# Kernel tuning notes

Measured on AMD Instinct MI355X. Metric: run time of the kernel, lower is better.

## Reference

```python
import jax, jax.numpy as jnp
import numpy as np

D, H, DK, L, FF = 512, 8, 64, 6, 2048
MAXREL = 512
R = 2 * MAXREL + 1
B, S = 4, 512


def _ln(x, g, b):
    m = jnp.mean(x, -1, keepdims=True)
    v = jnp.mean((x - m) ** 2, -1, keepdims=True)
    return (x - m) * jax.lax.rsqrt(v + 1e-5) * g + b


def _gelu(x):
    return jax.nn.gelu(x, approximate=False)


def setup_inputs() -> dict:
    key = jax.random.key(0)
    ks = iter(jax.random.split(key, 64))
    def rnd(shape, scale=0.02):
        return jax.random.normal(next(ks), shape, jnp.float32) * scale
    inp = {"x": jax.random.normal(next(ks), (B, S, D), jnp.float32)}
    # SeasonalDecomposition params (3 seasonal nets stacked on leading axis)
    inp.update(
        sd_t1_w=rnd((D, D)), sd_t1_b=jnp.zeros((D,), jnp.float32),
        sd_t2_w=rnd((D, D)), sd_t2_b=jnp.zeros((D,), jnp.float32),
        sd_s1_w=rnd((3, D, D // 2)), sd_s1_b=jnp.zeros((3, D // 2), jnp.float32),
        sd_s2_w=rnd((3, D // 2, D)), sd_s2_b=jnp.zeros((3, D), jnp.float32),
        sd_r1_w=rnd((D, D // 2)), sd_r1_b=jnp.zeros((D // 2,), jnp.float32),
        sd_r2_w=rnd((D // 2, D)), sd_r2_b=jnp.zeros((D,), jnp.float32),
        sd_comb=jnp.ones((5,), jnp.float32),
        # 6 TemporalFusionTransformer layers, params stacked on leading axis L
        wq=rnd((L, D, D)), wk=rnd((L, D, D)), wv=rnd((L, D, D)),
        wo_w=rnd((L, D, D)), wo_b=jnp.zeros((L, D), jnp.float32),
        rel_k=rnd((L, R, DK), 1.0), rel_v=rnd((L, R, DK), 1.0),
        ln_attn_g=jnp.ones((L, D), jnp.float32), ln_attn_b=jnp.zeros((L, D), jnp.float32),
        ff1_w=rnd((L, D, FF)), ff1_b=jnp.zeros((L, FF), jnp.float32),
        ff2_w=rnd((L, FF, D)), ff2_b=jnp.zeros((L, D), jnp.float32),
        n1_g=jnp.ones((L, D), jnp.float32), n1_b=jnp.zeros((L, D), jnp.float32),
        n2_g=jnp.ones((L, D), jnp.float32), n2_b=jnp.zeros((L, D), jnp.float32),
    )
    return inp


def _forward(x, sd_t1_w, sd_t1_b, sd_t2_w, sd_t2_b, sd_s1_w, sd_s1_b, sd_s2_w, sd_s2_b,
             sd_r1_w, sd_r1_b, sd_r2_w, sd_r2_b, sd_comb,
             wq, wk, wv, wo_w, wo_b, rel_k, rel_v, ln_attn_g, ln_attn_b,
             ff1_w, ff1_b, ff2_w, ff2_b, n1_g, n1_b, n2_g, n2_b):
    b, s, d = x.shape
    # relative position index matrix, rp[i, j] = clip(j - i) + MAXREL
    r = jnp.arange(s)
    rp = jnp.clip(r[None, :] - r[:, None], -MAXREL, MAXREL) + MAXREL  # [S, S]

    # ---- SeasonalDecomposition (eval mode: dropout = identity) ----
    trend = _gelu(x @ sd_t1_w + sd_t1_b) @ sd_t2_w + sd_t2_b
    h = _gelu(jnp.einsum('bsd,kdm->kbsm', x, sd_s1_w) + sd_s1_b[:, None, None, :])
    seas = jnp.einsum('kbsm,kmd->kbsd', h, sd_s2_w) + sd_s2_b[:, None, None, :]  # [3,B,S,D]
    resid = _gelu(x @ sd_r1_w + sd_r1_b) @ sd_r2_w + sd_r2_b
    w = jax.nn.softmax(sd_comb)
    x = w[0] * trend + w[4] * resid + jnp.einsum('k,kbsd->bsd', w[1:4], seas)

    scale = np.float32(1.0 / np.sqrt(DK))

    def layer(xc, p):
        q = (xc @ p['wq']).reshape(b, s, H, DK).transpose(0, 2, 1, 3)  # [B,H,S,DK]
        k = (xc @ p['wk']).reshape(b, s, H, DK).transpose(0, 2, 1, 3)
        v = (xc @ p['wv']).reshape(b, s, H, DK).transpose(0, 2, 1, 3)
        scores = jnp.einsum('bhid,bhjd->bhij', q, k) * scale
        rk = p['rel_k'][rp]  # [S,S,DK] gathered rel-pos key bias
        scores = scores + jnp.einsum('bhid,ijd->bhij', q, rk)
        a = jax.nn.softmax(scores, axis=-1)
        ctx = jnp.einsum('bhij,bhjd->bhid', a, v)
        rv = p['rel_v'][rp]  # [S,S,DK]
        ctx = ctx + jnp.einsum('bhij,ijd->bhid', a, rv)
        ctx = ctx.transpose(0, 2, 1, 3).reshape(b, s, d)
        out = ctx @ p['wo_w'] + p['wo_b']
        attn = _ln(out + xc, p['ln_attn_g'], p['ln_attn_b'])
        y = _ln(xc + attn, p['n1_g'], p['n1_b'])
        ff = _gelu(y @ p['ff1_w'] + p['ff1_b']) @ p['ff2_w'] + p['ff2_b']
        y = _ln(y + ff, p['n2_g'], p['n2_b'])
        return y, None

    layers = dict(wq=wq, wk=wk, wv=wv, wo_w=wo_w, wo_b=wo_b, rel_k=rel_k, rel_v=rel_v,
                  ln_attn_g=ln_attn_g, ln_attn_b=ln_attn_b,
                  ff1_w=ff1_w, ff1_b=ff1_b, ff2_w=ff2_w, ff2_b=ff2_b,
                  n1_g=n1_g, n1_b=n1_b, n2_g=n2_g, n2_b=n2_b)
    x, _ = jax.lax.scan(layer, x, layers)
    return x


def reference(x, sd_t1_w, sd_t1_b, sd_t2_w, sd_t2_b, sd_s1_w, sd_s1_b, sd_s2_w, sd_s2_b,
              sd_r1_w, sd_r1_b, sd_r2_w, sd_r2_b, sd_comb,
              wq, wk, wv, wo_w, wo_b, rel_k, rel_v, ln_attn_g, ln_attn_b,
              ff1_w, ff1_b, ff2_w, ff2_b, n1_g, n1_b, n2_g, n2_b):
    return _forward(x, sd_t1_w, sd_t1_b, sd_t2_w, sd_t2_b, sd_s1_w, sd_s1_b, sd_s2_w, sd_s2_b,
                    sd_r1_w, sd_r1_b, sd_r2_w, sd_r2_b, sd_comb,
                    wq, wk, wv, wo_w, wo_b, rel_k, rel_v, ln_attn_g, ln_attn_b,
                    ff1_w, ff1_b, ff2_w, ff2_b, n1_g, n1_b, n2_g, n2_b)
```

## Files before the change

kernel.cpp:

```cpp
#include <hip/hip_runtime.h>
#include <hip/hip_bf16.h>

typedef __attribute__((ext_vector_type(4))) float f32x4;
typedef __attribute__((ext_vector_type(8))) short bf16x8;
typedef __attribute__((ext_vector_type(4))) short bf16x4;

#define NL 6

static __device__ __forceinline__ unsigned short f2bf(float f) {
    __hip_bfloat16 h = __float2bfloat16(f);
    return *reinterpret_cast<unsigned short*>(&h);
}
static __device__ __forceinline__ float bf2f(unsigned short u) {
    union { unsigned int u32; float f; } c; c.u32 = ((unsigned int)u) << 16; return c.f;
}
static __device__ __forceinline__ float gelu_exact(float v) {
    return 0.5f * v * (1.0f + erff(v * 0.70710678118654752f));
}
static __device__ __forceinline__ void gload_lds16(const void* g, void* l) {
    __builtin_amdgcn_global_load_lds((const __attribute__((address_space(1))) void*)g,
                                     (__attribute__((address_space(3))) void*)l, 16, 0, 0);
}
static __device__ __forceinline__ f32x4 MF(bf16x8 a, bf16x8 b, f32x4 c) {
    return __builtin_amdgcn_mfma_f32_16x16x32_bf16(a, b, c, 0, 0, 0);
}

template<int BM, int BN, bool OBF, bool BIAS, bool GACT, bool SPART, bool DUAL, bool VTR>
__global__ __launch_bounds__(256)
void gemm3(const unsigned short* __restrict__ A, const unsigned short* __restrict__ B,
           void* __restrict__ C, unsigned short* __restrict__ C2,
           const float* __restrict__ bias,
           int M, int N, int nkt, int skN, int lda, int ldb, int ldc, float alpha,
           int modA, long sA1, long sA2, int modB, long sB1, long sB2,
           int modC, long sC1, long sC2, int biasStride, long pStride)
{
    constexpr int MI = BM / 32, NI = BN / 32;
    constexpr int ACH = BM / 8, NCH = (BM + BN) / 8;
    constexpr int HALF = (BM + BN) * 64;
    __shared__ __attribute__((aligned(16))) unsigned short Ls[2 * HALF];

    const int bz = blockIdx.z;
    const int sk = SPART ? (bz % skN) : 0;
    const int z  = SPART ? (bz / skN) : bz;
    const unsigned short* Ab = A + (long)(z % modA) * sA1 + (long)(z / modA) * sA2;
    const unsigned short* Bb = B + (long)(z % modB) * sB1 + (long)(z / modB) * sB2;
    const long offC = (long)(z % modC) * sC1 + (long)(z / modC) * sC2;

    const int bm0 = blockIdx.x * BM, bn0 = blockIdx.y * BN;
    const int t = threadIdx.x, lane = t & 63, w = t >> 6;
    const int wm = (w >> 1) * (BM / 2), wn = (w & 1) * (BN / 2);
    const int crow8 = lane >> 3, cs8 = lane & 7;
    const int fr = lane & 15, kq = lane >> 4;
    const int kBase = sk * nkt * 64;

    auto stagef = [&](int kt, int sb) {
        const int k0 = kBase + (kt << 6);
        const int base = sb * HALF;
        #pragma unroll
        for (int c0 = 0; c0 < NCH; c0 += 4) {
            int c = c0 + w;
            if (c < NCH) {
                const unsigned short* gp;
                if (c < ACH) {
                    int rit = c * 8 + crow8;
                    int ks = cs8 ^ (rit & 7);
                    gp = Ab + (long)(bm0 + rit) * lda + k0 + ks * 8;
                } else {
                    int rit = (c - ACH) * 8 + crow8;
                    int ks = cs8 ^ (rit & 7);
                    gp = Bb + (long)(bn0 + rit) * ldb + k0 + ks * 8;
                }
                gload_lds16(gp, &Ls[base + c * 512]);
            }
        }
    };

    f32x4 acc[MI][NI];
    #pragma unroll
    for (int a = 0; a < MI; a++)
        #pragma unroll
        for (int b = 0; b < NI; b++) acc[a][b] = (f32x4){0.f, 0.f, 0.f, 0.f};

    stagef(0, 0);
    __syncthreads();

    for (int kt = 0; kt < nkt; ++kt) {
        const int sb = kt & 1;
        const int base = sb * HALF;
        if (kt + 1 < nkt) stagef(kt + 1, sb ^ 1);
        bf16x8 af[2][MI], bfr[2][NI];
        #pragma unroll
        for (int mi = 0; mi < MI; mi++) {
            int R = wm + mi * 16 + fr;
            af[0][mi] = *(const bf16x8*)&Ls[base + R * 64 + ((kq ^ (R & 7)) << 3)];
            af[1][mi] = *(const bf16x8*)&Ls[base + R * 64 + (((4 + kq) ^ (R & 7)) << 3)];
        }
        #pragma unroll
        for (int ni = 0; ni < NI; ni++) {
            int Rb = wn + ni * 16 + fr;
            bfr[0][ni] = *(const bf16x8*)&Ls[base + BM * 64 + Rb * 64 + ((kq ^ (Rb & 7)) << 3)];
            bfr[1][ni] = *(const bf16x8*)&Ls[base + BM * 64 + Rb * 64 + (((4 + kq) ^ (Rb & 7)) << 3)];
        }
        #pragma unroll
        for (int kh = 0; kh < 2; kh++)
            #pragma unroll
            for (int mi = 0; mi < MI; mi++)
                #pragma unroll
                for (int ni = 0; ni < NI; ni++)
                    acc[mi][ni] = MF(af[kh][mi], bfr[kh][ni], acc[mi][ni]);
        __syncthreads();
    }

    const int q4 = (lane >> 4) << 2;
    if (VTR && bn0 >= 1024) {
        #pragma unroll
        for (int mi = 0; mi < MI; mi++)
            #pragma unroll
            for (int ni = 0; ni < NI; ni++)
                #pragma unroll
                for (int j = 0; j < 4; j++) {
                    int lr = wm + mi * 16 + q4 + j;
                    int lc = wn + ni * 16 + fr;
                    Ls[lc * 64 + ((((lr >> 4) ^ (lc & 3)) << 4) | (lr & 15))] = f2bf(acc[mi][ni][j]);
                }
        __syncthreads();
        int dl = t >> 2, c4 = (t & 3) << 4;
        const unsigned short* src = &Ls[dl * 64 + (((t & 3) ^ (dl & 3)) << 4)];
        unsigned short* dst = C2 + ((long)((bm0 >> 9) * 8 + ((bn0 - 1024) >> 6)) * 64 + dl) * 512
                              + (bm0 & 511) + c4;
        *(bf16x8*)dst = *(const bf16x8*)src;
        *((bf16x8*)dst + 1) = *((const bf16x8*)src + 1);
    } else if (SPART) {
        float* P = (float*)C + sk * pStride + offC;
        #pragma unroll
        for (int mi = 0; mi < MI; mi++)
            #pragma unroll
            for (int ni = 0; ni < NI; ni++)
                #pragma unroll
                for (int j = 0; j < 4; j++) {
                    int gr = bm0 + wm + mi * 16 + q4 + j;
                    int gc = bn0 + wn + ni * 16 + fr;
                    if (gc < N) P[(long)gr * ldc + gc] = acc[mi][ni][j] * alpha;
                }
    } else {
        float* Cf = (float*)C + offC;
        unsigned short* Ch = (unsigned short*)C + offC;
        unsigned short* C2h = DUAL ? (C2 + offC) : nullptr;
        const float* bp = BIAS ? (bias + (long)z * biasStride) : nullptr;
        #pragma unroll
        for (int mi = 0; mi < MI; mi++)
            #pragma unroll
            for (int ni = 0; ni < NI; ni++)
                #pragma unroll
                for (int j = 0; j < 4; j++) {
                    int gr = bm0 + wm + mi * 16 + q4 + j;
                    int gc = bn0 + wn + ni * 16 + fr;
                    if (gc < N) {
                        float v = acc[mi][ni][j] * alpha;
                        if (BIAS) v += bp[gc];
                        if (GACT) v = gelu_exact(v);
                        if (OBF) Ch[(long)gr * ldc + gc] = f2bf(v);
                        else     Cf[(long)gr * ldc + gc] = v;
                        if (DUAL) C2h[(long)gr * ldc + gc] = f2bf(v);
                    }
                }
    }
}

__global__ __launch_bounds__(256)
void fused_attn4(const unsigned short* __restrict__ qkv,
                 const unsigned short* __restrict__ vt,
                 const unsigned short* __restrict__ rk,
                 const unsigned short* __restrict__ rvt,
                 float* __restrict__ op, float* __restrict__ ml)
{
    __shared__ __attribute__((aligned(16))) unsigned short L[40960];
    const int bh = blockIdx.y, b = bh >> 3, h = bh & 7;
    const int i0 = blockIdx.x * 64;
    const int half = blockIdx.z;
    const int t = threadIdx.x, lane = t & 63, wv = t >> 6;
    const int crow = lane >> 2, cs = lane & 3;
    const int fr = lane & 15, kq = lane >> 4;
    const int q4 = kq << 2;
    const int iiw = wv * 16;
    const int PB = 28672, GA = 32768;

    const unsigned short* Qg = qkv + ((long)(b * 512 + i0)) * 1536 + h * 64;
    const unsigned short* Kg = qkv + ((long)(b * 512)) * 1536 + 512 + h * 64;
    const unsigned short* Vg = vt + ((long)bh * 64) * 512;

    auto stage = [&](int jt) {
        const int j0 = jt * 64, rbase = j0 - i0 + 448;
        #pragma unroll
        for (int k = 0; k < 12; k++) {
            int c = wv + k * 4;
            const unsigned short* gp; int dst;
            if (c < 8) {
                int kt = c >> 2, row = (c & 3) * 16 + crow, ks = cs ^ (row & 3);
                gp = Kg + (long)(j0 + row) * 1536 + kt * 32 + ks * 8;
                dst = 4096 + c * 512;
            } else if (c < 16) {
                int cc = c - 8;
                int kt = cc >> 2, row = (cc & 3) * 16 + crow, ks = cs ^ (row & 3);
                gp = Vg + (long)row * 512 + j0 + kt * 32 + ks * 8;
                dst = 8192 + cc * 512;
            } else if (c < 32) {
                int cc = c - 16;
                int kt = cc >> 2, row = (cc & 3) * 16 + crow, ks = cs ^ (row & 3);
                gp = rvt + (long)row * 1056 + rbase + kt * 32 + ks * 8;
                dst = 12288 + cc * 512;
            } else {
                int cc = c - 32;
                int kt = cc >> 3, row = (cc & 7) * 16 + crow, ks = cs ^ (row & 3);
                gp = rk + (long)(rbase + row) * 64 + kt * 32 + ks * 8;
                dst = 20480 + cc * 512;
            }
            gload_lds16(gp, &L[dst]);
        }
    };

    #pragma unroll
    for (int k = 0; k < 2; k++) {
        int c = wv + k * 4;
        int kt = c >> 2, row = (c & 3) * 16 + crow, ks = cs ^ (row & 3);
        gload_lds16(Qg + (long)row * 1536 + kt * 32 + ks * 8, &L[c * 512]);
    }
    stage(half * 4);
    __syncthreads();
    bf16x8 qf[2];
    {
        int r = iiw + fr;
        qf[0] = *(const bf16x8*)&L[r * 32 + ((kq ^ (r & 3)) << 3)];
        qf[1] = *(const bf16x8*)&L[2048 + r * 32 + ((kq ^ (r & 3)) << 3)];
    }

    f32x4 ctxa[4];
    #pragma unroll
    for (int ni = 0; ni < 4; ni++) ctxa[ni] = (f32x4){0.f, 0.f, 0.f, 0.f};
    float m_[4] = {-1e30f, -1e30f, -1e30f, -1e30f};
    float l_[4] = {0.f, 0.f, 0.f, 0.f};

    for (int q = 0; q < 4; ++q) {
        const int jt = half * 4 + q;
        f32x4 gacc[8];
        #pragma unroll
        for (int wb = 0; wb < 8; wb++) {
            int Rb = wb * 16 + fr;
            bf16x8 rk0 = *(const bf16x8*)&L[20480 + Rb * 32 + ((kq ^ (Rb & 3)) << 3)];
            bf16x8 rk1 = *(const bf16x8*)&L[24576 + Rb * 32 + ((kq ^ (Rb & 3)) << 3)];
            f32x4 g = (f32x4){0.f, 0.f, 0.f, 0.f};
            g = MF(qf[0], rk0, g);
            gacc[wb] = MF(qf[1], rk1, g);
        }
        #pragma unroll
        for (int wb = 0; wb < 8; wb++)
            #pragma unroll
            for (int j = 0; j < 4; j++) {
                int il = iiw + q4 + j, ww = wb * 16 + fr;
                L[GA + il * 128 + (((ww >> 3) ^ (il & 7)) << 3) + (ww & 7)] = f2bf(gacc[wb][j]);
            }
        f32x4 s[4];
        #pragma unroll
        for (int ni = 0; ni < 4; ni++) {
            int rB = ni * 16 + fr;
            bf16x8 b0 = *(const bf16x8*)&L[4096 + rB * 32 + ((kq ^ (rB & 3)) << 3)];
            bf16x8 b1 = *(const bf16x8*)&L[6144 + rB * 32 + ((kq ^ (rB & 3)) << 3)];
            f32x4 a0 = (f32x4){0.f, 0.f, 0.f, 0.f};
            a0 = MF(qf[0], b0, a0);
            s[ni] = MF(qf[1], b1, a0);
        }
        #pragma unroll
        for (int ni = 0; ni < 4; ni++)
            #pragma unroll
            for (int j = 0; j < 4; j++) {
                int il = iiw + q4 + j;
                int ww = ni * 16 + fr - il + 64;
                s[ni][j] = s[ni][j] * 0.125f
                         + bf2f(L[GA + il * 128 + (((ww >> 3) ^ (il & 7)) << 3) + (ww & 7)]);
            }
        float mx[4];
        #pragma unroll
        for (int j = 0; j < 4; j++) {
            mx[j] = fmaxf(fmaxf(s[0][j], s[1][j]), fmaxf(s[2][j], s[3][j]));
            #pragma unroll
            for (int msk = 1; msk < 16; msk <<= 1) mx[j] = fmaxf(mx[j], __shfl_xor(mx[j], msk));
        }
        float scl[4];
        #pragma unroll
        for (int j = 0; j < 4; j++) {
            float mn = fmaxf(m_[j], mx[j]);
            scl[j] = __expf(m_[j] - mn);
            m_[j] = mn;
        }
        float rs[4] = {0.f, 0.f, 0.f, 0.f};
        #pragma unroll
        for (int ni = 0; ni < 4; ni++)
            #pragma unroll
            for (int j = 0; j < 4; j++) {
                float p = __expf(s[ni][j] - m_[j]);
                s[ni][j] = p;
                rs[j] += p;
            }
        #pragma unroll
        for (int j = 0; j < 4; j++) {
            #pragma unroll
            for (int msk = 1; msk < 16; msk <<= 1) rs[j] += __shfl_xor(rs[j], msk);
            l_[j] = l_[j] * scl[j] + rs[j];
        }
        #pragma unroll
        for (int ni = 0; ni < 4; ni++)
            #pragma unroll
            for (int j = 0; j < 4; j++) ctxa[ni][j] *= scl[j];
        #pragma unroll
        for (int ni = 0; ni < 4; ni++)
            #pragma unroll
            for (int j = 0; j < 4; j++) {
                int il = iiw + q4 + j;
                int jj = ni * 16 + fr;
                unsigned short pb = f2bf(s[ni][j]);
                L[PB + il * 64 + (((jj >> 3) ^ (il & 7)) << 3) + (jj & 7)] = pb;
                int wI = jj - il + 64;
                L[GA + il * 128 + (((wI >> 3) ^ (il & 7)) << 3) + (wI & 7)] = pb;
                int wz = (wI + 64) & 127;
                L[GA + il * 128 + (((wz >> 3) ^ (il & 7)) << 3) + (wz & 7)] = 0;
            }
        const int r = iiw + fr;
        bf16x8 pa0 = *(const bf16x8*)&L[PB + r * 64 + ((kq ^ (r & 7)) << 3)];
        bf16x8 pa1 = *(const bf16x8*)&L[PB + r * 64 + (((4 + kq) ^ (r & 7)) << 3)];
        #pragma unroll
        for (int ni = 0; ni < 4; ni++) {
            int rB = ni * 16 + fr;
            bf16x8 vb0 = *(const bf16x8*)&L[8192 + rB * 32 + ((kq ^ (rB & 3)) << 3)];
            bf16x8 vb1 = *(const bf16x8*)&L[10240 + rB * 32 + ((kq ^ (rB & 3)) << 3)];
            ctxa[ni] = MF(pa0, vb0, ctxa[ni]);
            ctxa[ni] = MF(pa1, vb1, ctxa[ni]);
        }
        #pragma unroll
        for (int kt2 = 0; kt2 < 4; kt2++) {
            bf16x8 aa = *(const bf16x8*)&L[GA + r * 128 + (((kt2 * 4 + kq) ^ (r & 7)) << 3)];
            #pragma unroll
            for (int ni = 0; ni < 4; ni++) {
                int rB = ni * 16 + fr;
                bf16x8 rb = *(const bf16x8*)&L[12288 + kt2 * 2048 + rB * 32 + ((kq ^ (rB & 3)) << 3)];
                ctxa[ni] = MF(aa, rb, ctxa[ni]);
            }
        }
        if (q < 3) {
            __syncthreads();
            stage(jt + 1);
            __syncthreads();
        }
    }
    const long prow_base = (long)half * 16384 + (long)bh * 512 + i0;
    #pragma unroll
    for (int j = 0; j < 4; j++) {
        int il = iiw + q4 + j;
        long prow = prow_base + il;
        float* opr = op + prow * 64;
        #pragma unroll
        for (int ni = 0; ni < 4; ni++)
            opr[ni * 16 + fr] = ctxa[ni][j];
        if (fr == 0) {
            ml[prow * 2] = m_[j];
            ml[prow * 2 + 1] = l_[j];
        }
    }
}

__global__ __launch_bounds__(256)
void attn_merge(const float* __restrict__ op, const float* __restrict__ ml,
                unsigned short* __restrict__ ctx)
{
    const int wv = threadIdx.x >> 6, lane = threadIdx.x & 63;
    const long row = (long)blockIdx.x * 4 + wv;
    const int bh = (int)(row >> 9), i = (int)(row & 511);
    const int b = bh >> 3, h = bh & 7;
    float m0 = ml[row * 2], l0 = ml[row * 2 + 1];
    float m1 = ml[(row + 16384) * 2], l1 = ml[(row + 16384) * 2 + 1];
    float m = fmaxf(m0, m1);
    float a0 = __expf(m0 - m), a1 = __expf(m1 - m);
    float inv = 1.f / (l0 * a0 + l1 * a1);
    float o0 = op[row * 64 + lane];
    float o1 = op[(row + 16384) * 64 + lane];
    ctx[((long)(b * 512 + i)) * 512 + h * 64 + lane] = f2bf((o0 * a0 + o1 * a1) * inv);
}

__global__ __launch_bounds__(256)
void trcast_k(const float* __restrict__ in, unsigned short* __restrict__ out,
              int R, int C, int ldo, long inStride, long outStride,
              const float* __restrict__ scp, int sczs)
{
    __shared__ unsigned short tile[32][33];
    const int z = blockIdx.z;
    const float* ip = in + (long)z * inStride;
    unsigned short* op = out + (long)z * outStride;
    const float sc = scp ? scp[z * sczs] : 1.0f;
    const int c0 = blockIdx.x * 32, r0 = blockIdx.y * 32;
    const int tx = threadIdx.x & 31, ty = threadIdx.x >> 5;
    #pragma unroll
    for (int q = 0; q < 4; q++) {
        int r = r0 + ty + q * 8;
        float v = (r < R) ? ip[(long)r * C + c0 + tx] * sc : 0.f;
        tile[ty + q * 8][tx] = f2bf(v);
    }
    __syncthreads();
    #pragma unroll
    for (int q = 0; q < 4; q++) {
        int c = c0 + ty + q * 8;
        op[(long)c * ldo + r0 + tx] = tile[tx][ty + q * 8];
    }
}

__global__ __launch_bounds__(256)
void qkvwo_tr(const float* __restrict__ wq, const float* __restrict__ wk,
              const float* __restrict__ wv, const float* __restrict__ wo,
              unsigned short* __restrict__ qkvT, unsigned short* __restrict__ woT)
{
    __shared__ unsigned short tile[32][33];
    const int z = blockIdx.z;
    const int wsel = z / 6, l = z % 6;
    const float* ip = (wsel == 0 ? wq : wsel == 1 ? wk : wsel == 2 ? wv : wo) + (long)l * 262144;
    unsigned short* op = (wsel < 3) ? (qkvT + (long)l * 786432 + (long)wsel * 262144)
                                    : (woT + (long)l * 262144);
    const int c0 = blockIdx.x * 32, r0 = blockIdx.y * 32;
    const int tx = threadIdx.x & 31, ty = threadIdx.x >> 5;
    #pragma unroll
    for (int q = 0; q < 4; q++)
        tile[ty + q * 8][tx] = f2bf(ip[(long)(r0 + ty + q * 8) * 512 + c0 + tx]);
    __syncthreads();
    #pragma unroll
    for (int q = 0; q < 4; q++)
        op[(long)(c0 + ty + q * 8) * 512 + r0 + tx] = tile[tx][ty + q * 8];
}

__global__ __launch_bounds__(256)
void castpad_k(const float* __restrict__ in, unsigned short* __restrict__ out,
               int R, int C, long inStride, long outStride, long nPerZ)
{
    const int z = blockIdx.z;
    for (long idx = (long)blockIdx.x * 256 + threadIdx.x; idx < nPerZ;
         idx += (long)gridDim.x * 256) {
        int r = (int)(idx / C);
        float v = (r < R) ? in[(long)z * inStride + idx] : 0.f;
        out[(long)z * outStride + idx] = f2bf(v);
    }
}

__global__ __launch_bounds__(256)
void ln2x_k(const float* __restrict__ p0, const float* __restrict__ p1,
            const float* __restrict__ wb, const float* __restrict__ x,
            const float* __restrict__ g1, const float* __restrict__ b1,
            const float* __restrict__ g2, const float* __restrict__ b2,
            float* __restrict__ yf, unsigned short* __restrict__ yb)
{
    const int wv = threadIdx.x >> 6, lane = threadIdx.x & 63;
    const long row = (long)blockIdx.x * 4 + wv;
    const int base = lane * 8;
    const float* pa = p0 + row * 512 + base;
    const float* pbp = p1 + row * 512 + base;
    const float* px = x + row * 512 + base;
    float xv[8], v[8];
    {
        float4 x0 = *(const float4*)px, x1 = *(const float4*)(px + 4);
        float4 a0 = *(const float4*)pa, a1 = *(const float4*)(pa + 4);
        float4 c0 = *(const float4*)pbp, c1 = *(const float4*)(pbp + 4);
        float4 w0 = *(const float4*)(wb + base), w1 = *(const float4*)(wb + base + 4);
        xv[0] = x0.x; xv[1] = x0.y; xv[2] = x0.z; xv[3] = x0.w;
        xv[4] = x1.x; xv[5] = x1.y; xv[6] = x1.z; xv[7] = x1.w;
        v[0] = xv[0] + a0.x + c0.x + w0.x; v[1] = xv[1] + a0.y + c0.y + w0.y;
        v[2] = xv[2] + a0.z + c0.z + w0.z; v[3] = xv[3] + a0.w + c0.w + w0.w;
        v[4] = xv[4] + a1.x + c1.x + w1.x; v[5] = xv[5] + a1.y + c1.y + w1.y;
        v[6] = xv[6] + a1.z + c1.z + w1.z; v[7] = xv[7] + a1.w + c1.w + w1.w;
    }
    float s = 0.f;
    #pragma unroll
    for (int jj = 0; jj < 8; jj++) s += v[jj];
    #pragma unroll
    for (int off = 32; off; off >>= 1) s += __shfl_xor(s, off);
    float mean = s * (1.f / 512.f);
    float vs = 0.f;
    #pragma unroll
    for (int jj = 0; jj < 8; jj++) { float d = v[jj] - mean; vs += d * d; }
    #pragma unroll
    for (int off = 32; off; off >>= 1) vs += __shfl_xor(vs, off);
    float inv = rsqrtf(vs * (1.f / 512.f) + 1e-5f);
    float4 ga = *(const float4*)(g1 + base), gb = *(const float4*)(g1 + base + 4);
    float4 ba = *(const float4*)(b1 + base), bb = *(const float4*)(b1 + base + 4);
    float gg[8] = {ga.x, ga.y, ga.z, ga.w, gb.x, gb.y, gb.z, gb.w};
    float ee[8] = {ba.x, ba.y, ba.z, ba.w, bb.x, bb.y, bb.z, bb.w};
    float tvec[8];
    #pragma unroll
    for (int jj = 0; jj < 8; jj++) tvec[jj] = xv[jj] + (v[jj] - mean) * inv * gg[jj] + ee[jj];
    float s2 = 0.f;
    #pragma unroll
    for (int jj = 0; jj < 8; jj++) s2 += tvec[jj];
    #pragma unroll
    for (int off = 32; off; off >>= 1) s2 += __shfl_xor(s2, off);
    float m2 = s2 * (1.f / 512.f);
    float vs2 = 0.f;
    #pragma unroll
    for (int jj = 0; jj < 8; jj++) { float d = tvec[jj] - m2; vs2 += d * d; }
    #pragma unroll
    for (int off = 32; off; off >>= 1) vs2 += __shfl_xor(vs2, off);
    float inv2 = rsqrtf(vs2 * (1.f / 512.f) + 1e-5f);
    float4 gc = *(const float4*)(g2 + base), gd = *(const float4*)(g2 + base + 4);
    float4 bc = *(const float4*)(b2 + base), bd = *(const float4*)(b2 + base + 4);
    float g2v[8] = {gc.x, gc.y, gc.z, gc.w, gd.x, gd.y, gd.z, gd.w};
    float b2v[8] = {bc.x, bc.y, bc.z, bc.w, bd.x, bd.y, bd.z, bd.w};
    float r[8];
    #pragma unroll
    for (int jj = 0; jj < 8; jj++) r[jj] = (tvec[jj] - m2) * inv2 * g2v[jj] + b2v[jj];
    float* pf = yf + row * 512 + base;
    *(float4*)pf = (float4){r[0], r[1], r[2], r[3]};
    *(float4*)(pf + 4) = (float4){r[4], r[5], r[6], r[7]};
    bf16x8 ov;
    #pragma unroll
    for (int jj = 0; jj < 8; jj++) ov[jj] = (short)f2bf(r[jj]);
    *(bf16x8*)(yb + row * 512 + base) = ov;
}

__global__ __launch_bounds__(256)
void lnff_k(const float* __restrict__ y1, const float* __restrict__ parts,
            const float* __restrict__ bias,
            const float* __restrict__ g, const float* __restrict__ be,
            float* __restrict__ o, unsigned short* __restrict__ ob)
{
    const int wv = threadIdx.x >> 6, lane = threadIdx.x & 63;
    const long row = (long)blockIdx.x * 4 + wv;
    const int base = lane * 8;
    const float* pa = y1 + row * 512 + base;
    float v[8];
    {
        float4 x0 = *(const float4*)pa, x1 = *(const float4*)(pa + 4);
        float4 w0 = *(const float4*)(bias + base), w1 = *(const float4*)(bias + base + 4);
        v[0] = x0.x + w0.x; v[1] = x0.y + w0.y; v[2] = x0.z + w0.z; v[3] = x0.w + w0.w;
        v[4] = x1.x + w1.x; v[5] = x1.y + w1.y; v[6] = x1.z + w1.z; v[7] = x1.w + w1.w;
    }
    #pragma unroll
    for (int k = 0; k < 4; k++) {
        const float* pp = parts + (long)k * 1048576 + row * 512 + base;
        float4 a0 = *(const float4*)pp, a1 = *(const float4*)(pp + 4);
        v[0] += a0.x; v[1] += a0.y; v[2] += a0.z; v[3] += a0.w;
        v[4] += a1.x; v[5] += a1.y; v[6] += a1.z; v[7] += a1.w;
    }
    float s = 0.f;
    #pragma unroll
    for (int jj = 0; jj < 8; jj++) s += v[jj];
    #pragma unroll
    for (int off = 32; off; off >>= 1) s += __shfl_xor(s, off);
    float mean = s * (1.f / 512.f);
    float vs = 0.f;
    #pragma unroll
    for (int jj = 0; jj < 8; jj++) { float d = v[jj] - mean; vs += d * d; }
    #pragma unroll
    for (int off = 32; off; off >>= 1) vs += __shfl_xor(vs, off);
    float inv = rsqrtf(vs * (1.f / 512.f) + 1e-5f);
    float4 g0 = *(const float4*)(g + base), g1 = *(const float4*)(g + base + 4);
    float4 e0 = *(const float4*)(be + base), e1 = *(const float4*)(be + base + 4);
    float gg[8] = {g0.x, g0.y, g0.z, g0.w, g1.x, g1.y, g1.z, g1.w};
    float ee[8] = {e0.x, e0.y, e0.z, e0.w, e1.x, e1.y, e1.z, e1.w};
    float r[8];
    #pragma unroll
    for (int jj = 0; jj < 8; jj++) r[jj] = (v[jj] - mean) * inv * gg[jj] + ee[jj];
    float* po = o + row * 512 + base;
    *(float4*)po = (float4){r[0], r[1], r[2], r[3]};
    *(float4*)(po + 4) = (float4){r[4], r[5], r[6], r[7]};
    bf16x8 ov;
    #pragma unroll
    for (int jj = 0; jj < 8; jj++) ov[jj] = (short)f2bf(r[jj]);
    *(bf16x8*)(ob + row * 512 + base) = ov;
}

__global__ void softmax5_k(const float* __restrict__ comb, float* __restrict__ c5)
{
    if (threadIdx.x == 0 && blockIdx.x == 0) {
        float c[5]; float m = -1e30f;
        for (int k = 0; k < 5; k++) { c[k] = comb[k]; m = fmaxf(m, c[k]); }
        float s = 0.f;
        for (int k = 0; k < 5; k++) { c[k] = __expf(c[k] - m); s += c[k]; }
        for (int k = 0; k < 5; k++) c5[k] = c[k] / s;
    }
}

__global__ __launch_bounds__(256)
void bias_build_k(const float* __restrict__ t1b, const float* __restrict__ r1b,
                  const float* __restrict__ s1b, const float* __restrict__ t2b,
                  const float* __restrict__ r2b, const float* __restrict__ s2b,
                  const float* __restrict__ c5, float* __restrict__ b1c,
                  float* __restrict__ bc)
{
    int i = threadIdx.x + blockIdx.x * 256;
    if (i < 512) b1c[i] = t1b[i];
    else if (i < 768) b1c[i] = r1b[i - 512];
    else if (i < 1536) b1c[i] = s1b[i - 768];
    else if (i < 2048) {
        int n = i - 1536;
        bc[n] = c5[0] * t2b[n] + c5[4] * r2b[n]
              + c5[1] * s2b[n] + c5[2] * s2b[512 + n] + c5[3] * s2b[1024 + n];
    }
}

#define G3(BM,BN,OBF,BIAS,GACT,SPART,DUAL,VTR, A,B,C,C2,bias_, M,N,NKT,SKN, lda,ldb,ldc, alpha, mA,a1,a2, mB,b1,b2, mC,c1,c2, bstr, pstr, Zg) \
    gemm3<BM,BN,OBF,BIAS,GACT,SPART,DUAL,VTR><<<dim3((M)/(BM), ((N)+(BN)-1)/(BN), (Zg)), dim3(256), 0, stream>>>( \
        (A),(B),(C),(C2),(bias_),(M),(N),(NKT),(SKN),(lda),(ldb),(ldc),(alpha), \
        (mA),(long)(a1),(long)(a2),(mB),(long)(b1),(long)(b2),(mC),(long)(c1),(long)(c2),(bstr),(long)(pstr))

extern "C" void kernel_launch(void* const* d_in, const int* in_sizes, int n_in,
                              void* d_out, int out_size, void* d_ws, size_t ws_size,
                              hipStream_t stream)
{
    (void)in_sizes; (void)n_in; (void)out_size; (void)ws_size;
    const float* x    = (const float*)d_in[0];
    const float* t1w  = (const float*)d_in[1];
    const float* t1b  = (const float*)d_in[2];
    const float* t2w  = (const float*)d_in[3];
    const float* t2b  = (const float*)d_in[4];
    const float* s1w  = (const float*)d_in[5];
    const float* s1b  = (const float*)d_in[6];
    const float* s2w  = (const float*)d_in[7];
    const float* s2b  = (const float*)d_in[8];
    const float* r1w  = (const float*)d_in[9];
    const float* r1b  = (const float*)d_in[10];
    const float* r2w  = (const float*)d_in[11];
    const float* r2b  = (const float*)d_in[12];
    const float* comb = (const float*)d_in[13];
    const float* wq   = (const float*)d_in[14];
    const float* wk   = (const float*)d_in[15];
    const float* wvv  = (const float*)d_in[16];
    const float* wow  = (const float*)d_in[17];
    const float* wob  = (const float*)d_in[18];
    const float* relk = (const float*)d_in[19];
    const float* relv = (const float*)d_in[20];
    const float* lag  = (const float*)d_in[21];
    const float* labi = (const float*)d_in[22];
    const float* f1w  = (const float*)d_in[23];
    const float* f1b  = (const float*)d_in[24];
    const float* f2w  = (const float*)d_in[25];
    const float* f2b  = (const float*)d_in[26];
    const float* n1g  = (const float*)d_in[27];
    const float* n1b  = (const float*)d_in[28];
    const float* n2g  = (const float*)d_in[29];
    const float* n2b  = (const float*)d_in[30];

    char* ws = (char*)d_ws;
    #define OFFK(kb) (ws + (size_t)(kb) * 1024)
    float* X    = (float*)OFFK(0);
    float* T3   = (float*)OFFK(8192);
    float* PART = (float*)OFFK(12288);
    float* OP   = PART;
    float* ML   = PART + 2097152;
    unsigned short* Xb   = (unsigned short*)OFFK(45056);
    unsigned short* Xb0  = (unsigned short*)OFFK(47104);
    unsigned short* QKVb = (unsigned short*)OFFK(49152);
    unsigned short* VT   = (unsigned short*)OFFK(55296);
    unsigned short* CTXb = (unsigned short*)OFFK(57344);
    unsigned short* T3b  = (unsigned short*)OFFK(59392);
    unsigned short* FFb  = (unsigned short*)OFFK(61440);
    unsigned short* W1   = (unsigned short*)OFFK(69632);
    unsigned short* W2   = (unsigned short*)OFFK(71168);
    float* b1c = (float*)OFFK(72704);
    float* bc  = (float*)OFFK(72712);
    float* c5  = (float*)OFFK(72716);
    unsigned short* qkvT = (unsigned short*)OFFK(119808);
    unsigned short* woT  = (unsigned short*)OFFK(129024);
    unsigned short* f1wT = (unsigned short*)OFFK(132096);
    unsigned short* f2wT = (unsigned short*)OFFK(144384);
    unsigned short* relkb= (unsigned short*)OFFK(156672);
    unsigned short* rvT  = (unsigned short*)OFFK(157488);
    unsigned short* Hb   = QKVb;

    castpad_k<<<dim3(1024, 1, 1), 256, 0, stream>>>(x, Xb0, 2048, 512, 1048576, 1048576, 1048576);
    softmax5_k<<<dim3(1), 64, 0, stream>>>(comb, c5);
    bias_build_k<<<dim3(8), 256, 0, stream>>>(t1b, r1b, s1b, t2b, r2b, s2b, c5, b1c, bc);
    trcast_k<<<dim3(16, 16, 1), 256, 0, stream>>>(t1w, W1, 512, 512, 512, 0, 0, nullptr, 0);
    trcast_k<<<dim3(8, 16, 1), 256, 0, stream>>>(r1w, W1 + 262144, 512, 256, 512, 0, 0, nullptr, 0);
    trcast_k<<<dim3(8, 16, 3), 256, 0, stream>>>(s1w, W1 + 393216, 512, 256, 512, 131072, 131072, nullptr, 0);
    trcast_k<<<dim3(16, 16, 1), 256, 0, stream>>>(t2w, W2, 512, 512, 1536, 0, 0, c5, 0);
    trcast_k<<<dim3(16, 8, 1), 256, 0, stream>>>(r2w, W2 + 512, 256, 512, 1536, 0, 0, c5 + 4, 0);
    trcast_k<<<dim3(16, 8, 3), 256, 0, stream>>>(s2w, W2 + 768, 256, 512, 1536, 131072, 256, c5 + 1, 1);
    qkvwo_tr<<<dim3(16, 16, 24), 256, 0, stream>>>(wq, wk, wvv, wow, qkvT, woT);
    trcast_k<<<dim3(64, 16, 6), 256, 0, stream>>>(f1w, f1wT, 512, 2048, 512, 1048576, 1048576, nullptr, 0);
    trcast_k<<<dim3(16, 64, 6), 256, 0, stream>>>(f2w, f2wT, 2048, 512, 2048, 1048576, 1048576, nullptr, 0);
    trcast_k<<<dim3(2, 33, 6), 256, 0, stream>>>(relv, rvT, 1025, 64, 1056, 65600, 67584, nullptr, 0);
    castpad_k<<<dim3(272, 1, 6), 256, 0, stream>>>(relk, relkb, 1025, 64, 65600, 69632, 69632);

    G3(64,64,true,true,true,false,false,false,  Xb0, W1, Hb, nullptr, b1c, 2048,1536,8,1, 512,512,1536, 1.f,
       1,0,0, 1,0,0, 1,0,0, 0,0, 1);
    G3(64,64,false,true,false,false,true,false, Hb, W2, X, Xb, bc, 2048,512,24,1, 1536,1536,512, 1.f,
       1,0,0, 1,0,0, 1,0,0, 0,0, 1);

    for (int l = 0; l < NL; ++l) {
        const unsigned short* qkvTl = qkvT + (long)l * 786432;
        const unsigned short* woTl  = woT + (long)l * 262144;
        const unsigned short* f1Tl  = f1wT + (long)l * 1048576;
        const unsigned short* f2Tl  = f2wT + (long)l * 1048576;
        const unsigned short* rkl   = relkb + (long)l * 69632;
        const unsigned short* rvl   = rvT + (long)l * 67584;

        G3(64,64,true,false,false,false,false,true, Xb, qkvTl, QKVb, VT, nullptr, 2048,1536,8,1, 512,512,1536, 1.f,
           1,0,0, 1,0,0, 1,0,0, 0,0, 1);
        fused_attn4<<<dim3(8, 32, 2), 256, 0, stream>>>(QKVb, VT, rkl, rvl, OP, ML);
        attn_merge<<<dim3(4096), 256, 0, stream>>>(OP, ML, CTXb);
        G3(64,64,false,false,false,true,false,false, CTXb, woTl, PART, nullptr, nullptr, 2048,512,4,2, 512,512,512, 1.f,
           1,0,0, 1,0,0, 1,0,0, 0,1048576, 2);
        ln2x_k<<<dim3(512), 256, 0, stream>>>(PART, PART + 1048576, wob + l * 512, X,
                                              lag + l * 512, labi + l * 512,
                                              n1g + l * 512, n1b + l * 512, T3, T3b);
        G3(64,64,true,true,true,false,false,false, T3b, f1Tl, FFb, nullptr, f1b + l * 2048, 2048,2048,8,1, 512,512,2048, 1.f,
           1,0,0, 1,0,0, 1,0,0, 0,0, 1);
        G3(64,64,false,false,false,true,false,false, FFb, f2Tl, PART, nullptr, nullptr, 2048,512,8,4, 2048,2048,512, 1.f,
           1,0,0, 1,0,0, 1,0,0, 0,1048576, 4);
        float* outp = (l == NL - 1) ? (float*)d_out : X;
        lnff_k<<<dim3(512), 256, 0, stream>>>(T3, PART, f2b + l * 512,
                                              n2g + l * 512, n2b + l * 512, outp, Xb);
    }
}
```

Before: 551.4 us.

## Fuse split-KV attention merge into attention kernel via atomic counter; merge weight-prep launches

The attention kernel now bumps a per-tile atomic counter after writing its partial output and softmax stats. The second of the two split-KV halves to finish combines both partials and writes the bf16 context directly, which removes the separate attn_merge launch each layer. Separately, the six weight transpose-cast launches and the bias build are folded into one wprep_k launch, and the sync counters are zeroed with a memset. The merge step now runs serially at the tail of only half the blocks and depends on threadfence ordering for correctness.

Result: slower. 969.6 us (+75.8%).

```diff
diff --git a/kernel.cpp b/kernel.cpp
--- a/kernel.cpp
+++ b/kernel.cpp
@@ -168,13 +168,15 @@
 }
 
 __global__ __launch_bounds__(256)
-void fused_attn4(const unsigned short* __restrict__ qkv,
+void fused_attn5(const unsigned short* __restrict__ qkv,
                  const unsigned short* __restrict__ vt,
                  const unsigned short* __restrict__ rk,
                  const unsigned short* __restrict__ rvt,
-                 float* __restrict__ op, float* __restrict__ ml)
+                 float* __restrict__ op, float* __restrict__ ml,
+                 unsigned int* __restrict__ sync, unsigned short* __restrict__ ctx)
 {
     __shared__ __attribute__((aligned(16))) unsigned short L[40960];
+    __shared__ unsigned int oldS;
     const int bh = blockIdx.y, b = bh >> 3, h = bh & 7;
     const int i0 = blockIdx.x * 64;
     const int half = blockIdx.z;
@@ -365,24 +367,27 @@
             ml[prow * 2 + 1] = l_[j];
         }
     }
-}
-
-__global__ __launch_bounds__(256)
-void attn_merge(const float* __restrict__ op, const float* __restrict__ ml,
-                unsigned short* __restrict__ ctx)
-{
-    const int wv = threadIdx.x >> 6, lane = threadIdx.x & 63;
-    const long row = (long)blockIdx.x * 4 + wv;
-    const int bh = (int)(row >> 9), i = (int)(row & 511);
-    const int b = bh >> 3, h = bh & 7;
-    float m0 = ml[row * 2], l0 = ml[row * 2 + 1];
-    float m1 = ml[(row + 16384) * 2], l1 = ml[(row + 16384) * 2 + 1];
-    float m = fmaxf(m0, m1);
-    float a0 = __expf(m0 - m), a1 = __expf(m1 - m);
-    float inv = 1.f / (l0 * a0 + l1 * a1);
-    float o0 = op[row * 64 + lane];
-    float o1 = op[(row + 16384) * 64 + lane];
-    ctx[((long)(b * 512 + i)) * 512 + h * 64 + lane] = f2bf((o0 * a0 + o1 * a1) * inv);
+    __syncthreads();
+    __threadfence();
+    if (t == 0) oldS = atomicAdd(&sync[blockIdx.x * 32 + bh], 1u);
+    __syncthreads();
+    if (oldS == 1) {
+        __threadfence();
+        const long r0g = (long)bh * 512 + i0;
+        for (int e = t; e < 4096; e += 256) {
+            int r = e >> 6, d = e & 63;
+            long row = r0g + r;
+            float m0 = ml[row * 2], l0 = ml[row * 2 + 1];
+            float m1 = ml[(row + 16384) * 2], l1 = ml[(row + 16384) * 2 + 1];
+            float m = fmaxf(m0, m1);
+            float a0 = __expf(m0 - m), a1 = __expf(m1 - m);
+            float inv = 1.f / (l0 * a0 + l1 * a1);
+            float o0 = op[row * 64 + d];
+            float o1 = op[(row + 16384) * 64 + d];
+            ctx[((long)(b * 512 + i0 + r)) * 512 + h * 64 + d] = f2bf((o0 * a0 + o1 * a1) * inv);
+        }
+        if (t == 0) atomicExch(&sync[blockIdx.x * 32 + bh], 0u);
+    }
 }
 
 __global__ __launch_bounds__(256)
@@ -431,6 +436,59 @@
     #pragma unroll
     for (int q = 0; q < 4; q++)
         op[(long)(c0 + ty + q * 8) * 512 + r0 + tx] = tile[tx][ty + q * 8];
+}
+
+__global__ __launch_bounds__(256)
+void wprep_k(const float* __restrict__ t1w, const float* __restrict__ r1w,
+             const float* __restrict__ s1w, const float* __restrict__ t2w,
+             const float* __restrict__ r2w, const float* __restrict__ s2w,
+             const float* __restrict__ c5,
+             unsigned short* __restrict__ W1, unsigned short* __restrict__ W2,
+             const float* __restrict__ t1b, const float* __restrict__ r1b,
+             const float* __restrict__ s1b, const float* __restrict__ t2b,
+             const float* __restrict__ r2b, const float* __restrict__ s2b,
+             float* __restrict__ b1c, float* __restrict__ bc)
+{
+    const int z = blockIdx.z;
+    if (z == 10) {
+        int i = threadIdx.x + blockIdx.x * 256;
+        if (blockIdx.y != 0 || blockIdx.x >= 8) return;
+        if (i < 512) b1c[i] = t1b[i];
+        else if (i < 768) b1c[i] = r1b[i - 512];
+        else if (i < 1536) b1c[i] = s1b[i - 768];
+        else if (i < 2048) {
+            int n = i - 1536;
+            bc[n] = c5[0] * t2b[n] + c5[4] * r2b[n]
+                  + c5[1] * s2b[n] + c5[2] * s2b[512 + n] + c5[3] * s2b[1024 + n];
+        }
+        return;
+    }
+    const float* ip; unsigned short* op;
+    int R, C, ldo; float sc = 1.0f;
+    if (z == 0)      { ip = t1w; op = W1; R = 512; C = 512; ldo = 512; }
+    else if (z == 1) { ip = r1w; op = W1 + 262144; R = 512; C = 256; ldo = 512; }
+    else if (z <= 4) { int k = z - 2; ip = s1w + (long)k * 131072; op = W1 + 393216 + (long)k * 131072;
+                       R = 512; C = 256; ldo = 512; }
+    else if (z == 5) { ip = t2w; op = W2; R = 512; C = 512; ldo = 1536; sc = c5[0]; }
+    else if (z == 6) { ip = r2w; op = W2 + 512; R = 256; C = 512; ldo = 1536; sc = c5[4]; }
+    else             { int k = z - 7; ip = s2w + (long)k * 131072; op = W2 + 768 + (long)k * 256;
+                       R = 256; C = 512; ldo = 1536; sc = c5[1 + k]; }
+    const int c0 = blockIdx.x * 32, r0 = blockIdx.y * 32;
+    if (c0 >= C || r0 >= R) return;
+    __shared__ unsigned short tile[32][33];
+    const int tx = threadIdx.x & 31, ty = threadIdx.x >> 5;
+    #pragma unroll
+    for (int q = 0; q < 4; q++) {
+        int r = r0 + ty + q * 8;
+        float v = (r < R) ? ip[(long)r * C + c0 + tx] * sc : 0.f;
+        tile[ty + q * 8][tx] = f2bf(v);
+    }
+    __syncthreads();
+    #pragma unroll
+    for (int q = 0; q < 4; q++) {
+        int c = c0 + ty + q * 8;
+        op[(long)c * ldo + r0 + tx] = tile[tx][ty + q * 8];
+    }
 }
 
 __global__ __launch_bounds__(256)
@@ -579,24 +637,6 @@
         float s = 0.f;
         for (int k = 0; k < 5; k++) { c[k] = __expf(c[k] - m); s += c[k]; }
         for (int k = 0; k < 5; k++) c5[k] = c[k] / s;
-    }
-}
-
-__global__ __launch_bounds__(256)
-void bias_build_k(const float* __restrict__ t1b, const float* __restrict__ r1b,
-                  const float* __restrict__ s1b, const float* __restrict__ t2b,
-                  const float* __restrict__ r2b, const float* __restrict__ s2b,
-                  const float* __restrict__ c5, float* __restrict__ b1c,
-                  float* __restrict__ bc)
-{
-    int i = threadIdx.x + blockIdx.x * 256;
-    if (i < 512) b1c[i] = t1b[i];
-    else if (i < 768) b1c[i] = r1b[i - 512];
-    else if (i < 1536) b1c[i] = s1b[i - 768];
-    else if (i < 2048) {
-        int n = i - 1536;
-        bc[n] = c5[0] * t2b[n] + c5[4] * r2b[n]
-              + c5[1] * s2b[n] + c5[2] * s2b[512 + n] + c5[3] * s2b[1024 + n];
     }
 }
 
@@ -661,6 +701,7 @@
     float* b1c = (float*)OFFK(72704);
     float* bc  = (float*)OFFK(72712);
     float* c5  = (float*)OFFK(72716);
+    unsigned int* SYNC = (unsigned int*)OFFK(72718);
     unsigned short* qkvT = (unsigned short*)OFFK(119808);
     unsigned short* woT  = (unsigned short*)OFFK(129024);
     unsigned short* f1wT = (unsigned short*)OFFK(132096);
@@ -669,15 +710,11 @@
     unsigned short* rvT  = (unsigned short*)OFFK(157488);
     unsigned short* Hb   = QKVb;
 
+    hipMemsetAsync(SYNC, 0, 1024, stream);
     castpad_k<<<dim3(1024, 1, 1), 256, 0, stream>>>(x, Xb0, 2048, 512, 1048576, 1048576, 1048576);
     softmax5_k<<<dim3(1), 64, 0, stream>>>(comb, c5);
-    bias_build_k<<<dim3(8), 256, 0, stream>>>(t1b, r1b, s1b, t2b, r2b, s2b, c5, b1c, bc);
-    trcast_k<<<dim3(16, 16, 1), 256, 0, stream>>>(t1w, W1, 512, 512, 512, 0, 0, nullptr, 0);
-    trcast_k<<<dim3(8, 16, 1), 256, 0, stream>>>(r1w, W1 + 262144, 512, 256, 512, 0, 0, nullptr, 0);
-    trcast_k<<<dim3(8, 16, 3), 256, 0, stream>>>(s1w, W1 + 393216, 512, 256, 512, 131072, 131072, nullptr, 0);
-    trcast_k<<<dim3(16, 16, 1), 256, 0, stream>>>(t2w, W2, 512, 512, 1536, 0, 0, c5, 0);
-    trcast_k<<<dim3(16, 8, 1), 256, 0, stream>>>(r2w, W2 + 512, 256, 512, 1536, 0, 0, c5 + 4, 0);
-    trcast_k<<<dim3(16, 8, 3), 256, 0, stream>>>(s2w, W2 + 768, 256, 512, 1536, 131072, 256, c5 + 1, 1);
+    wprep_k<<<dim3(16, 16, 11), 256, 0, stream>>>(t1w, r1w, s1w, t2w, r2w, s2w, c5, W1, W2,
+                                                  t1b, r1b, s1b, t2b, r2b, s2b, b1c, bc);
     qkvwo_tr<<<dim3(16, 16, 24), 256, 0, stream>>>(wq, wk, wvv, wow, qkvT, woT);
     trcast_k<<<dim3(64, 16, 6), 256, 0, stream>>>(f1w, f1wT, 512, 2048, 512, 1048576, 1048576, nullptr, 0);
     trcast_k<<<dim3(16, 64, 6), 256, 0, stream>>>(f2w, f2wT, 2048, 512, 2048, 1048576, 1048576, nullptr, 0);
@@ -699,8 +736,7 @@
 
         G3(64,64,true,false,false,false,false,true, Xb, qkvTl, QKVb, VT, nullptr, 2048,1536,8,1, 512,512,1536, 1.f,
            1,0,0, 1,0,0, 1,0,0, 0,0, 1);
-        fused_attn4<<<dim3(8, 32, 2), 256, 0, stream>>>(QKVb, VT, rkl, rvl, OP, ML);
-        attn_merge<<<dim3(4096), 256, 0, stream>>>(OP, ML, CTXb);
+        fused_attn5<<<dim3(8, 32, 2), 256, 0, stream>>>(QKVb, VT, rkl, rvl, OP, ML, SYNC, CTXb);
         G3(64,64,false,false,false,true,false,false, CTXb, woTl, PART, nullptr, nullptr, 2048,512,4,2, 512,512,512, 1.f,
            1,0,0, 1,0,0, 1,0,0, 0,1048576, 2);
         ln2x_k<<<dim3(512), 256, 0, stream>>>(PART, PART + 1048576, wob + l * 512, X,
```
